# Optimization experiments

Measured on AMD Instinct MI355X. Metric: run time of the kernel, lower is better.

The kernel has to match this reference:

```python
import jax, jax.numpy as jnp
import numpy as np

B, C, H8, W8 = 2, 256, 56, 96
RADIUS, LEVELS = 4, 4


def setup_inputs() -> dict:
    key = jax.random.key(0)
    k1, k2, k3, k4, k5 = jax.random.split(key, 5)
    fmap1 = jax.random.normal(k1, (B, C, H8, W8), jnp.float32)
    fmap2 = jax.random.normal(k2, (B, C, H8, W8), jnp.float32)
    xs = jnp.arange(W8, dtype=jnp.float32)
    ys = jnp.arange(H8, dtype=jnp.float32)
    bx, by = jnp.broadcast_arrays(xs[None, :], ys[:, None])
    base = jnp.stack([bx, by], axis=0)  # [2,H8,W8], x first (as create_coords_grid)
    coords = base[None] + 4.0 * jax.random.normal(k3, (B, 2, H8, W8), jnp.float32)
    flow = jax.random.normal(k4, (B, 2, H8, W8), jnp.float32)
    mask = jax.random.normal(k5, (B, 9 * 8 * 8, H8, W8), jnp.float32)
    return {"fmap1": fmap1, "fmap2": fmap2, "coords": coords, "flow": flow, "mask": mask}


def _bilinear_sample(cflat, Hl, Wl, px, py):
    # cflat: [N, Hl*Wl]; px,py: [N,P] pixel coords; zero padding outside (grid_sample default)
    x0 = jnp.floor(px)
    y0 = jnp.floor(py)
    wx = px - x0
    wy = py - y0
    x0 = x0.astype(jnp.int32)
    y0 = y0.astype(jnp.int32)

    def g(xi, yi):
        valid = (xi >= 0) & (xi <= Wl - 1) & (yi >= 0) & (yi <= Hl - 1)
        idx = jnp.clip(yi, 0, Hl - 1) * Wl + jnp.clip(xi, 0, Wl - 1)
        return jnp.where(valid, jnp.take_along_axis(cflat, idx, axis=1), 0.0)

    return ((1 - wy) * ((1 - wx) * g(x0, y0) + wx * g(x0 + 1, y0))
            + wy * ((1 - wx) * g(x0, y0 + 1) + wx * g(x0 + 1, y0 + 1)))


def _corr_lookup(fmap1, fmap2, coords):
    b, c, h, w = fmap1.shape
    n = b * h * w
    # all-pairs correlation, scaled by sqrt(C)
    corr = jnp.einsum('bchw,bcij->bhwij', fmap1, fmap2) / jnp.sqrt(jnp.float32(c))
    cl = corr.reshape(n, h, w)
    # query coords (pixel units at level 0)
    cx = coords[:, 0].reshape(n)
    cy = coords[:, 1].reshape(n)
    r = RADIUS
    lin = jnp.linspace(-r, r, 2 * r + 1, dtype=jnp.float32)
    # replicates torch.meshgrid(dy,dx) quirk: x-offset varies along axis 0, y along axis 1
    xo = jnp.repeat(lin, 2 * r + 1)  # [81]
    yo = jnp.tile(lin, 2 * r + 1)    # [81]
    outs = []
    for i in range(LEVELS):
        Hl, Wl = cl.shape[1], cl.shape[2]
        cflat = cl.reshape(n, Hl * Wl)
        px = cx[:, None] / (2 ** i) + xo[None, :]
        py = cy[:, None] / (2 ** i) + yo[None, :]
        samp = _bilinear_sample(cflat, Hl, Wl, px, py)  # [N,81]
        outs.append(samp.reshape(b, h, w, -1))
        if i < LEVELS - 1:  # 2x2 avg pool, stride 2
            cl = cl.reshape(n, Hl // 2, 2, Wl // 2, 2).mean(axis=(2, 4))
    out = jnp.concatenate(outs, axis=-1)  # [B,h,w,4*81]
    return out.transpose(0, 3, 1, 2)


def _convex_upsample(flow, mask):
    b, ch, h, w = flow.shape
    m = mask.reshape(b, 1, 9, 8, 8, h, w)
    m = jax.nn.softmax(m, axis=2)
    fp = jnp.pad(8.0 * flow, ((0, 0), (0, 0), (1, 1), (1, 1)))
    # 3x3 unfold, kernel positions row-major (matches F.unfold ordering)
    patches = jnp.stack([fp[:, :, i:i + h, j:j + w]
                         for i in range(3) for j in range(3)], axis=2)  # [B,2,9,h,w]
    up = jnp.sum(m * patches[:, :, :, None, None], axis=2)  # [B,2,8,8,h,w]
    up = up.transpose(0, 1, 4, 2, 5, 3)  # [B,2,h,8,w,8]
    return up.reshape(b, ch, 8 * h, 8 * w)


def reference(fmap1, fmap2, coords, flow, mask):
    corr_feats = _corr_lookup(fmap1, fmap2, coords)  # [B,324,H8,W8]
    up_flow = _convex_upsample(flow, mask)           # [B,2,8*H8,8*W8]
    return (corr_feats, up_flow)
```

## Files before the change

kernel.cpp:

```cpp
#include <hip/hip_runtime.h>
#include <math.h>

constexpr int B = 2, C = 256, H = 56, W = 96;
constexpr int HW = H * W;

#define SQ 21.166666f
constexpr float SCL = 36.0f / (127.0f * 127.0f * 16.0f);

constexpr size_t F1T_B = 0;
constexpr size_t L0_B  = (size_t)B * HW * C;
constexpr size_t L1_B  = L0_B + (size_t)B * HW * C;
constexpr size_t L2_B  = L1_B + (size_t)B * 28 * 48 * C;
constexpr size_t L3_B  = L2_B + (size_t)B * 14 * 24 * C;
constexpr size_t STG_B = L3_B + (size_t)B * 7 * 12 * C;
constexpr size_t OUT0_ELEMS = (size_t)B * 324 * HW;

static __device__ __forceinline__ int dot4acc(int a, int b, int c) {
#if __has_builtin(__builtin_amdgcn_sdot4)
    return __builtin_amdgcn_sdot4(a, b, c, false);
#else
    c += (int)(char)(a) * (int)(char)(b);
    c += (int)(char)(a >> 8) * (int)(char)(b >> 8);
    c += (int)(char)(a >> 16) * (int)(char)(b >> 16);
    c += (int)(char)(a >> 24) * (int)(char)(b >> 24);
    return c;
#endif
}

static __device__ __forceinline__ unsigned short pack_i8x2(float a, float b) {
    int ia = (int)rintf(a); ia = ia < -127 ? -127 : (ia > 127 ? 127 : ia);
    int ib = (int)rintf(b); ib = ib < -127 ? -127 : (ib > 127 ? 127 : ib);
    return (unsigned short)((ia & 0xFF) | ((ib & 0xFF) << 8));
}

__global__ void transpose_in(const float* __restrict__ fmap1,
                             const float* __restrict__ fmap2,
                             char* __restrict__ ws) {
    __shared__ float tile[64][33];
    int z = blockIdx.z;
    int b = z & 1, m = z >> 1;
    const float* src = m ? fmap2 : fmap1;
    unsigned short* dst = (unsigned short*)(ws + (m ? L0_B : F1T_B));
    int c0 = blockIdx.y * 64, q0 = blockIdx.x * 32;
    int tx = threadIdx.x, ty = threadIdx.y;
#pragma unroll
    for (int r = 0; r < 8; ++r) {
        int cl = ty + r * 8;
        tile[cl][tx] = src[((size_t)(b * C + c0 + cl)) * HW + q0 + tx];
    }
    __syncthreads();
#pragma unroll
    for (int r = 0; r < 4; ++r) {
        int pl = ty + r * 8;
        dst[((size_t)b * HW + q0 + pl) * 128 + (c0 >> 1) + tx] =
            pack_i8x2(tile[2 * tx][pl] * SQ, tile[2 * tx + 1][pl] * SQ);
    }
}

constexpr int NP1 = B * 28 * 48 * C / 2;
constexpr int NP2 = B * 14 * 24 * C / 2;
constexpr int NP3 = B * 7 * 12 * C / 2;
__global__ void build_pools(char* __restrict__ ws) {
    const unsigned short* L0p = (const unsigned short*)(ws + L0_B);
    int t = blockIdx.x * 256 + threadIdx.x;
    int l, tl;
    if (t < NP1)             { l = 1; tl = t; }
    else if (t < NP1 + NP2)  { l = 2; tl = t - NP1; }
    else                     { l = 3; tl = t - NP1 - NP2; }
    int Wo = W >> l, Ho = H >> l, S = 1 << l;
    int c2 = tl & 127;
    int r = tl >> 7;
    int x = r % Wo; r /= Wo;
    int y = r % Ho;
    int b = r / Ho;
    int sx = 0, sy = 0;
    for (int dy = 0; dy < S; ++dy)
        for (int dx = 0; dx < S; ++dx) {
            unsigned short v = L0p[((size_t)(b * H + y * S + dy) * W + x * S + dx) * 128 + c2];
            sx += (int)(char)(v & 0xFF);
            sy += (int)(char)(v >> 8);
        }
    float inv = 1.0f / (S * S);
    unsigned short* dst = (unsigned short*)(ws + (l == 1 ? L1_B : (l == 2 ? L2_B : L3_B)));
    dst[tl] = pack_i8x2((float)sx * inv, (float)sy * inv);
}

__global__ __launch_bounds__(256) void corr_lookup(
    const float* __restrict__ coords, const char* __restrict__ ws,
    _Float16* __restrict__ stage) {
    int q = blockIdx.x;
    int w = q % W;
    int t2 = q / W;
    int h = t2 % H;
    int b = t2 / H;
    int tid = threadIdx.x;

    __shared__ float Dsh[4][100];

    int wave = tid >> 6, lane = tid & 63, u = lane & 7, grp = lane >> 3;

    const int4* ap = (const int4*)(ws + F1T_B + ((size_t)b * HW + h * W + w) * C);
    int4 A0 = ap[2 * u], A1 = ap[2 * u + 1];

    int l = wave;
    int Hl = H >> l, Wl = W >> l;
    size_t off = (l == 0 ? L0_B : (l == 1 ? L1_B : (l == 2 ? L2_B : L3_B)));
    const char* base8 = ws + off + (size_t)b * Hl * Wl * C;

    float cx = coords[((size_t)(b * 2 + 0)) * HW + h * W + w];
    float cy = coords[((size_t)(b * 2 + 1)) * HW + h * W + w];
    float scale = 1.0f / (float)(1 << l);
    float fx = cx * scale, fy = cy * scale;
    float fxf = floorf(fx), fyf = floorf(fy);
    float wx = fx - fxf, wy = fy - fyf;
    int ix = (int)fxf, iy = (int)fyf;

    int xx = grp;
    int x = ix - 4 + grp;
    int y = iy - 4;

#pragma unroll
    for (int it = 0; it < 13; ++it) {
        bool live = (it < 12) | (grp < 4);
        int s = 0;
        if (live && (unsigned)x < (unsigned)Wl && (unsigned)y < (unsigned)Hl) {
            const int4* cp = (const int4*)(base8 + ((size_t)(y * Wl + x)) * C + u * 32);
            int4 c0 = cp[0], c1 = cp[1];
            s = dot4acc(c0.x, A0.x, s);
            s = dot4acc(c0.y, A0.y, s);
            s = dot4acc(c0.z, A0.z, s);
            s = dot4acc(c0.w, A0.w, s);
            s = dot4acc(c1.x, A1.x, s);
            s = dot4acc(c1.y, A1.y, s);
            s = dot4acc(c1.z, A1.z, s);
            s = dot4acc(c1.w, A1.w, s);
        }
        s += __shfl_xor(s, 1);
        s += __shfl_xor(s, 2);
        s += __shfl_xor(s, 4);
        if (u == 0 && live) Dsh[wave][it * 8 + grp] = (float)s * SCL;
        xx += 8;
        int carry = (xx >= 10);
        xx -= carry ? 10 : 0;
        x += carry ? -2 : 8;
        y += carry;
    }
    __syncthreads();

    size_t bse = ((size_t)b * HW + h * W + w) * 324 + l * 81;
    for (int o = lane; o < 81; o += 64) {
        int xo = o / 9;
        int yo = o - xo * 9;
        float v00 = Dsh[wave][yo * 10 + xo];
        float v01 = Dsh[wave][yo * 10 + xo + 1];
        float v10 = Dsh[wave][(yo + 1) * 10 + xo];
        float v11 = Dsh[wave][(yo + 1) * 10 + xo + 1];
        float s = (1.f - wy) * ((1.f - wx) * v00 + wx * v01)
                +        wy  * ((1.f - wx) * v10 + wx * v11);
        stage[bse + o] = (_Float16)s;
    }
}

constexpr int T_BLOCKS = 168 * 11 * B;
__global__ __launch_bounds__(256) void tail_kernel(
    const _Float16* __restrict__ stage, const float* __restrict__ flow,
    const float* __restrict__ mask, float* __restrict__ out0,
    float* __restrict__ out1) {
    __shared__ float smem[72 * 96 + 2 * 3 * 98];
    int blk = blockIdx.x;
    int tid = threadIdx.x;

    if (blk < T_BLOCKS) {
        float (*tile)[33] = (float(*)[33])smem;
        int b = blk / (168 * 11);
        int rem = blk % (168 * 11);
        int by = rem / 168, bx = rem % 168;
        int ch0 = by * 32, q0 = bx * 32;
        int tx = tid & 31, ty = tid >> 5;
#pragma unroll
        for (int r = 0; r < 4; ++r) {
            int pl = ty + r * 8;
            if (ch0 + tx < 324)
                tile[pl][tx] = (float)stage[((size_t)b * HW + q0 + pl) * 324 + ch0 + tx];
        }
        __syncthreads();
#pragma unroll
        for (int r = 0; r < 4; ++r) {
            int chl = ty + r * 8;
            if (ch0 + chl < 324)
                out0[((size_t)(b * 324 + ch0 + chl)) * HW + q0 + tx] = tile[tx][chl];
        }
        return;
    }

    float* msk = smem;
    float* fst = smem + 72 * 96;
    int cb = blk - T_BLOCKS;
    int i = cb & 7;
    int r = cb >> 3;
    int h = r % H;
    int b = r / H;

    for (int idx = tid; idx < 72 * 96; idx += 256) {
        int row = idx / 96, wc = idx - row * 96;
        int k = row >> 3, j = row & 7;
        int gl = k * 64 + i * 8 + j;
        msk[idx] = mask[((size_t)(b * 576 + gl)) * HW + h * W + wc];
    }
    for (int idx = tid; idx < 588; idx += 256) {
        int ch = idx / 294;
        int rem2 = idx - ch * 294;
        int rr = rem2 / 98;
        int xw = rem2 - rr * 98;
        int hh = h + rr - 1, ww = xw - 1;
        float v = 0.f;
        if (hh >= 0 && hh < H && ww >= 0 && ww < W)
            v = 8.0f * flow[((size_t)(b * 2 + ch)) * HW + hh * W + ww];
        fst[idx] = v;
    }
    __syncthreads();

#pragma unroll
    for (int rr = 0; rr < 3; ++rr) {
        int col = tid + rr * 256;
        int w = col >> 3, j = col & 7;
        float m[9], mx = -1e30f;
#pragma unroll
        for (int k = 0; k < 9; ++k) {
            m[k] = msk[(k * 8 + j) * 96 + w];
            mx = fmaxf(mx, m[k]);
        }
        float sum = 0.f;
#pragma unroll
        for (int k = 0; k < 9; ++k) {
            m[k] = __expf(m[k] - mx);
            sum += m[k];
        }
        float inv = 1.0f / sum;
        float a0 = 0.f, a1 = 0.f;
#pragma unroll
        for (int k = 0; k < 9; ++k) {
            int ki = k / 3, kj = k - ki * 3;
            float wgt = m[k] * inv;
            a0 = fmaf(wgt, fst[0 * 294 + ki * 98 + w + kj], a0);
            a1 = fmaf(wgt, fst[1 * 294 + ki * 98 + w + kj], a1);
        }
        size_t row8 = (size_t)8 * h + i;
        out1[((size_t)(b * 2 + 0) * 448 + row8) * 768 + col] = a0;
        out1[((size_t)(b * 2 + 1) * 448 + row8) * 768 + col] = a1;
    }
}

extern "C" void kernel_launch(void* const* d_in, const int* in_sizes, int n_in,
                              void* d_out, int out_size, void* d_ws, size_t ws_size,
                              hipStream_t stream) {
    const float* fmap1  = (const float*)d_in[0];
    const float* fmap2  = (const float*)d_in[1];
    const float* coords = (const float*)d_in[2];
    const float* flow   = (const float*)d_in[3];
    const float* maskp  = (const float*)d_in[4];
    float* out = (float*)d_out;
    char* ws = (char*)d_ws;
    _Float16* stage = (_Float16*)(ws + STG_B);

    transpose_in<<<dim3(HW / 32, C / 64, 2 * B), dim3(32, 8), 0, stream>>>(fmap1, fmap2, ws);
    build_pools<<<(NP1 + NP2 + NP3) / 256, 256, 0, stream>>>(ws);
    corr_lookup<<<B * HW, 256, 0, stream>>>(coords, ws, stage);
    tail_kernel<<<T_BLOCKS + B * H * 8, 256, 0, stream>>>(stage, flow, maskp, out, out + OUT0_ELEMS);
}
```

Baseline: 160.0 us.

## Fuse corr lookup with output transpose and merge upsample into prep kernel

The correlation lookup now handles 8 query pixels per block and writes the bilinear results straight to the channel-major output, so the fp16 staging buffer and its separate transpose pass are gone. Each query row is split across only 2 lanes with wide int4 loads and four independent dot accumulators. The convex upsample work moves into the same launch as the input transpose/quantize, and pool accumulation is unrolled per level through templates. Output writes are now 8 contiguous floats per channel, which are less coalesced than the old 32-wide tile transpose, and the block shared-memory footprint grows.

```diff
diff --git a/kernel.cpp b/kernel.cpp
--- a/kernel.cpp
+++ b/kernel.cpp
@@ -3,6 +3,7 @@
 
 constexpr int B = 2, C = 256, H = 56, W = 96;
 constexpr int HW = H * W;
+constexpr int RADIUS = 4;
 
 #define SQ 21.166666f
 constexpr float SCL = 36.0f / (127.0f * 127.0f * 16.0f);
@@ -12,7 +13,6 @@
 constexpr size_t L1_B  = L0_B + (size_t)B * HW * C;
 constexpr size_t L2_B  = L1_B + (size_t)B * 28 * 48 * C;
 constexpr size_t L3_B  = L2_B + (size_t)B * 14 * 24 * C;
-constexpr size_t STG_B = L3_B + (size_t)B * 7 * 12 * C;
 constexpr size_t OUT0_ELEMS = (size_t)B * 324 * HW;
 
 static __device__ __forceinline__ int dot4acc(int a, int b, int c) {
@@ -33,34 +33,117 @@
     return (unsigned short)((ia & 0xFF) | ((ib & 0xFF) << 8));
 }
 
-__global__ void transpose_in(const float* __restrict__ fmap1,
-                             const float* __restrict__ fmap2,
-                             char* __restrict__ ws) {
-    __shared__ float tile[64][33];
-    int z = blockIdx.z;
-    int b = z & 1, m = z >> 1;
-    const float* src = m ? fmap2 : fmap1;
-    unsigned short* dst = (unsigned short*)(ws + (m ? L0_B : F1T_B));
-    int c0 = blockIdx.y * 64, q0 = blockIdx.x * 32;
-    int tx = threadIdx.x, ty = threadIdx.y;
-#pragma unroll
-    for (int r = 0; r < 8; ++r) {
-        int cl = ty + r * 8;
-        tile[cl][tx] = src[((size_t)(b * C + c0 + cl)) * HW + q0 + tx];
+constexpr int TP_BLOCKS = (HW / 32) * (C / 64) * 2 * B;
+constexpr int CU_BLOCKS = B * H * 8;
+__global__ __launch_bounds__(256) void prep_kernel(
+    const float* __restrict__ fmap1, const float* __restrict__ fmap2,
+    const float* __restrict__ flow, const float* __restrict__ mask,
+    char* __restrict__ ws, float* __restrict__ out1) {
+    __shared__ float smem[72 * 96 + 2 * 3 * 98];
+    int bid = blockIdx.x;
+    int tid = threadIdx.x;
+
+    if (bid < TP_BLOCKS) {
+        float (*tile)[33] = (float(*)[33])smem;
+        int zi = bid / 672;
+        int rem = bid % 672;
+        int by = rem / 168, bx = rem % 168;
+        int b = zi & 1, m = zi >> 1;
+        const float* src = m ? fmap2 : fmap1;
+        unsigned short* dst = (unsigned short*)(ws + (m ? L0_B : F1T_B));
+        int c0 = by * 64, q0 = bx * 32;
+        int tx = tid & 31, ty = tid >> 5;
+#pragma unroll
+        for (int r = 0; r < 8; ++r) {
+            int cl = ty + r * 8;
+            tile[cl][tx] = src[((size_t)(b * C + c0 + cl)) * HW + q0 + tx];
+        }
+        __syncthreads();
+#pragma unroll
+        for (int r = 0; r < 4; ++r) {
+            int pl = ty + r * 8;
+            dst[((size_t)b * HW + q0 + pl) * 128 + (c0 >> 1) + tx] =
+                pack_i8x2(tile[2 * tx][pl] * SQ, tile[2 * tx + 1][pl] * SQ);
+        }
+        return;
+    }
+
+    float* msk = smem;
+    float* fst = smem + 72 * 96;
+    int cb = bid - TP_BLOCKS;
+    int i = cb & 7;
+    int r = cb >> 3;
+    int h = r % H;
+    int b = r / H;
+
+    for (int idx = tid; idx < 72 * 96; idx += 256) {
+        int row = idx / 96, wc = idx - row * 96;
+        int k = row >> 3, j = row & 7;
+        int gl = k * 64 + i * 8 + j;
+        msk[idx] = mask[((size_t)(b * 576 + gl)) * HW + h * W + wc];
+    }
+    for (int idx = tid; idx < 588; idx += 256) {
+        int ch = idx / 294;
+        int rem2 = idx - ch * 294;
+        int rr = rem2 / 98;
+        int xw = rem2 - rr * 98;
+        int hh = h + rr - 1, ww = xw - 1;
+        float v = 0.f;
+        if (hh >= 0 && hh < H && ww >= 0 && ww < W)
+            v = 8.0f * flow[((size_t)(b * 2 + ch)) * HW + hh * W + ww];
+        fst[idx] = v;
     }
     __syncthreads();
-#pragma unroll
-    for (int r = 0; r < 4; ++r) {
-        int pl = ty + r * 8;
-        dst[((size_t)b * HW + q0 + pl) * 128 + (c0 >> 1) + tx] =
-            pack_i8x2(tile[2 * tx][pl] * SQ, tile[2 * tx + 1][pl] * SQ);
+
+#pragma unroll
+    for (int rr = 0; rr < 3; ++rr) {
+        int col = tid + rr * 256;
+        int w = col >> 3, j = col & 7;
+        float m[9], mx = -1e30f;
+#pragma unroll
+        for (int k = 0; k < 9; ++k) {
+            m[k] = msk[(k * 8 + j) * 96 + w];
+            mx = fmaxf(mx, m[k]);
+        }
+        float sum = 0.f;
+#pragma unroll
+        for (int k = 0; k < 9; ++k) {
+            m[k] = __expf(m[k] - mx);
+            sum += m[k];
+        }
+        float inv = 1.0f / sum;
+        float a0 = 0.f, a1 = 0.f;
+#pragma unroll
+        for (int k = 0; k < 9; ++k) {
+            int ki = k / 3, kj = k - ki * 3;
+            float wgt = m[k] * inv;
+            a0 = fmaf(wgt, fst[0 * 294 + ki * 98 + w + kj], a0);
+            a1 = fmaf(wgt, fst[1 * 294 + ki * 98 + w + kj], a1);
+        }
+        size_t row8 = (size_t)8 * h + i;
+        out1[((size_t)(b * 2 + 0) * 448 + row8) * 768 + col] = a0;
+        out1[((size_t)(b * 2 + 1) * 448 + row8) * 768 + col] = a1;
     }
 }
 
 constexpr int NP1 = B * 28 * 48 * C / 2;
 constexpr int NP2 = B * 14 * 24 * C / 2;
 constexpr int NP3 = B * 7 * 12 * C / 2;
-__global__ void build_pools(char* __restrict__ ws) {
+
+template <int S>
+static __device__ __forceinline__ void pool_accum(const unsigned short* src,
+                                                  int& sx, int& sy) {
+#pragma unroll
+    for (int dy = 0; dy < S; ++dy)
+#pragma unroll
+        for (int dx = 0; dx < S; ++dx) {
+            unsigned short v = src[(size_t)dy * (W * 128) + dx * 128];
+            sx += (int)(char)(v & 0xFF);
+            sy += (int)(char)(v >> 8);
+        }
+}
+
+__global__ __launch_bounds__(256) void build_pools(char* __restrict__ ws) {
     const unsigned short* L0p = (const unsigned short*)(ws + L0_B);
     int t = blockIdx.x * 256 + threadIdx.x;
     int l, tl;
@@ -73,181 +156,127 @@
     int x = r % Wo; r /= Wo;
     int y = r % Ho;
     int b = r / Ho;
+    const unsigned short* src =
+        L0p + ((size_t)(b * H + y * S) * W + x * S) * 128 + c2;
     int sx = 0, sy = 0;
-    for (int dy = 0; dy < S; ++dy)
-        for (int dx = 0; dx < S; ++dx) {
-            unsigned short v = L0p[((size_t)(b * H + y * S + dy) * W + x * S + dx) * 128 + c2];
-            sx += (int)(char)(v & 0xFF);
-            sy += (int)(char)(v >> 8);
-        }
+    if (l == 1)      pool_accum<2>(src, sx, sy);
+    else if (l == 2) pool_accum<4>(src, sx, sy);
+    else             pool_accum<8>(src, sx, sy);
     float inv = 1.0f / (S * S);
     unsigned short* dst = (unsigned short*)(ws + (l == 1 ? L1_B : (l == 2 ? L2_B : L3_B)));
     dst[tl] = pack_i8x2((float)sx * inv, (float)sy * inv);
 }
 
-__global__ __launch_bounds__(256) void corr_lookup(
+__global__ __launch_bounds__(256) void corr_fused(
     const float* __restrict__ coords, const char* __restrict__ ws,
-    _Float16* __restrict__ stage) {
-    int q = blockIdx.x;
-    int w = q % W;
-    int t2 = q / W;
-    int h = t2 % H;
-    int b = t2 / H;
+    float* __restrict__ out0) {
+    __shared__ float Dsh[4][8][101];
+    __shared__ float Wxy[4][8][2];
+
     int tid = threadIdx.x;
-
-    __shared__ float Dsh[4][100];
-
-    int wave = tid >> 6, lane = tid & 63, u = lane & 7, grp = lane >> 3;
-
-    const int4* ap = (const int4*)(ws + F1T_B + ((size_t)b * HW + h * W + w) * C);
-    int4 A0 = ap[2 * u], A1 = ap[2 * u + 1];
-
-    int l = wave;
+    int l = tid >> 6;
+    int lane = tid & 63;
+    int u = lane & 1;
+    int half = lane >> 5;
+    int pr = (lane & 31) >> 1;
+
+    int g0 = blockIdx.x * 8;
+    int b = g0 / HW;
+    int hw0 = g0 - b * HW;
+
     int Hl = H >> l, Wl = W >> l;
     size_t off = (l == 0 ? L0_B : (l == 1 ? L1_B : (l == 2 ? L2_B : L3_B)));
     const char* base8 = ws + off + (size_t)b * Hl * Wl * C;
-
-    float cx = coords[((size_t)(b * 2 + 0)) * HW + h * W + w];
-    float cy = coords[((size_t)(b * 2 + 1)) * HW + h * W + w];
-    float scale = 1.0f / (float)(1 << l);
-    float fx = cx * scale, fy = cy * scale;
-    float fxf = floorf(fx), fyf = floorf(fy);
-    float wx = fx - fxf, wy = fy - fyf;
-    int ix = (int)fxf, iy = (int)fyf;
-
-    int xx = grp;
-    int x = ix - 4 + grp;
-    int y = iy - 4;
-
-#pragma unroll
-    for (int it = 0; it < 13; ++it) {
-        bool live = (it < 12) | (grp < 4);
-        int s = 0;
-        if (live && (unsigned)x < (unsigned)Wl && (unsigned)y < (unsigned)Hl) {
-            const int4* cp = (const int4*)(base8 + ((size_t)(y * Wl + x)) * C + u * 32);
-            int4 c0 = cp[0], c1 = cp[1];
-            s = dot4acc(c0.x, A0.x, s);
-            s = dot4acc(c0.y, A0.y, s);
-            s = dot4acc(c0.z, A0.z, s);
-            s = dot4acc(c0.w, A0.w, s);
-            s = dot4acc(c1.x, A1.x, s);
-            s = dot4acc(c1.y, A1.y, s);
-            s = dot4acc(c1.z, A1.z, s);
-            s = dot4acc(c1.w, A1.w, s);
-        }
-        s += __shfl_xor(s, 1);
-        s += __shfl_xor(s, 2);
-        s += __shfl_xor(s, 4);
-        if (u == 0 && live) Dsh[wave][it * 8 + grp] = (float)s * SCL;
-        xx += 8;
-        int carry = (xx >= 10);
-        xx -= carry ? 10 : 0;
-        x += carry ? -2 : 8;
-        y += carry;
+    float scale = (l == 0 ? 1.0f : (l == 1 ? 0.5f : (l == 2 ? 0.25f : 0.125f)));
+
+    int xo0 = pr < 10 ? pr : pr - 10;
+    int yo0 = pr < 10 ? 0 : 1;
+
+    const char* f1b = ws + F1T_B;
+
+#pragma unroll 1
+    for (int qi = 0; qi < 4; ++qi) {
+        int qr = qi * 2 + half;
+        int g = g0 + qr;
+
+        const char* ab = f1b + (size_t)g * C + (u << 4);
+        int4 A0 = *(const int4*)(ab);
+        int4 A1 = *(const int4*)(ab + 32);
+        int4 A2 = *(const int4*)(ab + 64);
+        int4 A3 = *(const int4*)(ab + 96);
+        int4 A4 = *(const int4*)(ab + 128);
+        int4 A5 = *(const int4*)(ab + 160);
+        int4 A6 = *(const int4*)(ab + 192);
+        int4 A7 = *(const int4*)(ab + 224);
+
+        float cx = coords[(size_t)(b * 2 + 0) * HW + hw0 + qr];
+        float cy = coords[(size_t)(b * 2 + 1) * HW + hw0 + qr];
+        float fx = cx * scale, fy = cy * scale;
+        float fxf = floorf(fx), fyf = floorf(fy);
+        float wx = fx - fxf, wy = fy - fyf;
+        int ix = (int)fxf, iy = (int)fyf;
+        if (pr == 0 && u == 0) { Wxy[l][qr][0] = wx; Wxy[l][qr][1] = wy; }
+
+        int xo = xo0, yo = yo0;
+#pragma unroll
+        for (int it = 0; it < 7; ++it) {
+            bool live = (it < 6) | (pr < 4);
+            int x = ix - RADIUS + xo;
+            int y = iy - RADIUS + yo;
+            int s0 = 0, s1 = 0, s2 = 0, s3 = 0;
+            if (live && (unsigned)x < (unsigned)Wl && (unsigned)y < (unsigned)Hl) {
+                const char* rp = base8 + (((size_t)(y * Wl + x)) << 8) + (u << 4);
+                int4 c0 = *(const int4*)(rp);
+                int4 c1 = *(const int4*)(rp + 32);
+                int4 c2 = *(const int4*)(rp + 64);
+                int4 c3 = *(const int4*)(rp + 96);
+                int4 c4 = *(const int4*)(rp + 128);
+                int4 c5 = *(const int4*)(rp + 160);
+                int4 c6 = *(const int4*)(rp + 192);
+                int4 c7 = *(const int4*)(rp + 224);
+                s0 = dot4acc(c0.x, A0.x, s0); s1 = dot4acc(c0.y, A0.y, s1);
+                s2 = dot4acc(c0.z, A0.z, s2); s3 = dot4acc(c0.w, A0.w, s3);
+                s0 = dot4acc(c1.x, A1.x, s0); s1 = dot4acc(c1.y, A1.y, s1);
+                s2 = dot4acc(c1.z, A1.z, s2); s3 = dot4acc(c1.w, A1.w, s3);
+                s0 = dot4acc(c2.x, A2.x, s0); s1 = dot4acc(c2.y, A2.y, s1);
+                s2 = dot4acc(c2.z, A2.z, s2); s3 = dot4acc(c2.w, A2.w, s3);
+                s0 = dot4acc(c3.x, A3.x, s0); s1 = dot4acc(c3.y, A3.y, s1);
+                s2 = dot4acc(c3.z, A3.z, s2); s3 = dot4acc(c3.w, A3.w, s3);
+                s0 = dot4acc(c4.x, A4.x, s0); s1 = dot4acc(c4.y, A4.y, s1);
+                s2 = dot4acc(c4.z, A4.z, s2); s3 = dot4acc(c4.w, A4.w, s3);
+                s0 = dot4acc(c5.x, A5.x, s0); s1 = dot4acc(c5.y, A5.y, s1);
+                s2 = dot4acc(c5.z, A5.z, s2); s3 = dot4acc(c5.w, A5.w, s3);
+                s0 = dot4acc(c6.x, A6.x, s0); s1 = dot4acc(c6.y, A6.y, s1);
+                s2 = dot4acc(c6.z, A6.z, s2); s3 = dot4acc(c6.w, A6.w, s3);
+                s0 = dot4acc(c7.x, A7.x, s0); s1 = dot4acc(c7.y, A7.y, s1);
+                s2 = dot4acc(c7.z, A7.z, s2); s3 = dot4acc(c7.w, A7.w, s3);
+            }
+            int s = (s0 + s1) + (s2 + s3);
+            s += __shfl_xor(s, 1);
+            if (u == 0 && live) Dsh[l][qr][it * 16 + pr] = (float)s * SCL;
+            xo += 6;
+            int cr = xo >= 10;
+            xo -= cr ? 10 : 0;
+            yo += 1 + cr;
+        }
     }
     __syncthreads();
 
-    size_t bse = ((size_t)b * HW + h * W + w) * 324 + l * 81;
-    for (int o = lane; o < 81; o += 64) {
-        int xo = o / 9;
-        int yo = o - xo * 9;
-        float v00 = Dsh[wave][yo * 10 + xo];
-        float v01 = Dsh[wave][yo * 10 + xo + 1];
-        float v10 = Dsh[wave][(yo + 1) * 10 + xo];
-        float v11 = Dsh[wave][(yo + 1) * 10 + xo + 1];
-        float s = (1.f - wy) * ((1.f - wx) * v00 + wx * v01)
-                +        wy  * ((1.f - wx) * v10 + wx * v11);
-        stage[bse + o] = (_Float16)s;
-    }
-}
-
-constexpr int T_BLOCKS = 168 * 11 * B;
-__global__ __launch_bounds__(256) void tail_kernel(
-    const _Float16* __restrict__ stage, const float* __restrict__ flow,
-    const float* __restrict__ mask, float* __restrict__ out0,
-    float* __restrict__ out1) {
-    __shared__ float smem[72 * 96 + 2 * 3 * 98];
-    int blk = blockIdx.x;
-    int tid = threadIdx.x;
-
-    if (blk < T_BLOCKS) {
-        float (*tile)[33] = (float(*)[33])smem;
-        int b = blk / (168 * 11);
-        int rem = blk % (168 * 11);
-        int by = rem / 168, bx = rem % 168;
-        int ch0 = by * 32, q0 = bx * 32;
-        int tx = tid & 31, ty = tid >> 5;
-#pragma unroll
-        for (int r = 0; r < 4; ++r) {
-            int pl = ty + r * 8;
-            if (ch0 + tx < 324)
-                tile[pl][tx] = (float)stage[((size_t)b * HW + q0 + pl) * 324 + ch0 + tx];
-        }
-        __syncthreads();
-#pragma unroll
-        for (int r = 0; r < 4; ++r) {
-            int chl = ty + r * 8;
-            if (ch0 + chl < 324)
-                out0[((size_t)(b * 324 + ch0 + chl)) * HW + q0 + tx] = tile[tx][chl];
-        }
-        return;
-    }
-
-    float* msk = smem;
-    float* fst = smem + 72 * 96;
-    int cb = blk - T_BLOCKS;
-    int i = cb & 7;
-    int r = cb >> 3;
-    int h = r % H;
-    int b = r / H;
-
-    for (int idx = tid; idx < 72 * 96; idx += 256) {
-        int row = idx / 96, wc = idx - row * 96;
-        int k = row >> 3, j = row & 7;
-        int gl = k * 64 + i * 8 + j;
-        msk[idx] = mask[((size_t)(b * 576 + gl)) * HW + h * W + wc];
-    }
-    for (int idx = tid; idx < 588; idx += 256) {
-        int ch = idx / 294;
-        int rem2 = idx - ch * 294;
-        int rr = rem2 / 98;
-        int xw = rem2 - rr * 98;
-        int hh = h + rr - 1, ww = xw - 1;
-        float v = 0.f;
-        if (hh >= 0 && hh < H && ww >= 0 && ww < W)
-            v = 8.0f * flow[((size_t)(b * 2 + ch)) * HW + hh * W + ww];
-        fst[idx] = v;
-    }
-    __syncthreads();
-
-#pragma unroll
-    for (int rr = 0; rr < 3; ++rr) {
-        int col = tid + rr * 256;
-        int w = col >> 3, j = col & 7;
-        float m[9], mx = -1e30f;
-#pragma unroll
-        for (int k = 0; k < 9; ++k) {
-            m[k] = msk[(k * 8 + j) * 96 + w];
-            mx = fmaxf(mx, m[k]);
-        }
-        float sum = 0.f;
-#pragma unroll
-        for (int k = 0; k < 9; ++k) {
-            m[k] = __expf(m[k] - mx);
-            sum += m[k];
-        }
-        float inv = 1.0f / sum;
-        float a0 = 0.f, a1 = 0.f;
-#pragma unroll
-        for (int k = 0; k < 9; ++k) {
-            int ki = k / 3, kj = k - ki * 3;
-            float wgt = m[k] * inv;
-            a0 = fmaf(wgt, fst[0 * 294 + ki * 98 + w + kj], a0);
-            a1 = fmaf(wgt, fst[1 * 294 + ki * 98 + w + kj], a1);
-        }
-        size_t row8 = (size_t)8 * h + i;
-        out1[((size_t)(b * 2 + 0) * 448 + row8) * 768 + col] = a0;
-        out1[((size_t)(b * 2 + 1) * 448 + row8) * 768 + col] = a1;
+    for (int o = tid; o < 324 * 8; o += 256) {
+        int q = o & 7, ch = o >> 3;
+        int lv = ch / 81;
+        int o81 = ch - lv * 81;
+        int xo = o81 / 9;
+        int yo = o81 - xo * 9;
+        float wxv = Wxy[lv][q][0], wyv = Wxy[lv][q][1];
+        const float* D = Dsh[lv][q];
+        float v00 = D[yo * 10 + xo];
+        float v01 = D[yo * 10 + xo + 1];
+        float v10 = D[yo * 10 + xo + 10];
+        float v11 = D[yo * 10 + xo + 11];
+        float res = (1.f - wyv) * ((1.f - wxv) * v00 + wxv * v01)
+                  +        wyv  * ((1.f - wxv) * v10 + wxv * v11);
+        out0[((size_t)(b * 324 + ch)) * HW + hw0 + q] = res;
     }
 }
 
@@ -261,10 +290,9 @@
     const float* maskp  = (const float*)d_in[4];
     float* out = (float*)d_out;
     char* ws = (char*)d_ws;
-    _Float16* stage = (_Float16*)(ws + STG_B);
-
-    transpose_in<<<dim3(HW / 32, C / 64, 2 * B), dim3(32, 8), 0, stream>>>(fmap1, fmap2, ws);
+
+    prep_kernel<<<TP_BLOCKS + CU_BLOCKS, 256, 0, stream>>>(
+        fmap1, fmap2, flow, maskp, ws, out + OUT0_ELEMS);
     build_pools<<<(NP1 + NP2 + NP3) / 256, 256, 0, stream>>>(ws);
-    corr_lookup<<<B * HW, 256, 0, stream>>>(coords, ws, stage);
-    tail_kernel<<<T_BLOCKS + B * H * 8, 256, 0, stream>>>(stage, flow, maskp, out, out + OUT0_ELEMS);
-}
+    corr_fused<<<B * HW / 8, 256, 0, stream>>>(coords, ws, out);
+}
```

Measured after the change: 175.5 us. 1.1x slower.
